# Optimization experiments

Measured on AMD Instinct MI355X. Metric: run time of the kernel, lower is better.

## Reference

```python
import jax, jax.numpy as jnp
import numpy as np

REPLACE = 4
REMAIN = 32
EPS = 1e-12


def _l2norm(x, axis):
    return x / jnp.maximum(jnp.linalg.norm(x, axis=axis, keepdims=True), EPS)


def setup_inputs() -> dict:
    key = jax.random.key(0)
    ks = jax.random.split(key, 16)
    B, d = 4096, 64
    n_users, n_entities, n_items = 100000, 200000, 50000
    K, n_cans, n_rel = 64, 64, 100
    return {
        "users": jax.random.randint(ks[0], (B,), 0, n_users),
        "items": jax.random.randint(ks[1], (B,), 0, n_items),
        "kg_neighbors": jax.random.randint(ks[2], (n_items, K), 0, n_entities),
        "all_candidates": jax.random.randint(ks[3], (n_rel, n_cans), 0, n_entities),
        "neighbor_relations": jax.random.randint(ks[4], (n_items, K), 0, n_rel),
        "user_all_embeddings": jax.random.normal(ks[5], (n_users, d), jnp.float32),
        "entity_all_embeddings": jax.random.normal(ks[6], (n_entities, d), jnp.float32),
        "item_embeddings": jax.random.normal(ks[7], (B, d), jnp.float32),
        "ui_W": jax.random.normal(ks[8], (2 * d, d), jnp.float32) / np.sqrt(2 * d),
        "ui_b": jnp.zeros((d,), jnp.float32),
        "e1_W": jax.random.normal(ks[9], (d, d), jnp.float32) / np.sqrt(d),
        "e1_b": jnp.zeros((d,), jnp.float32),
        "e2_W": jax.random.normal(ks[10], (d, d), jnp.float32) / np.sqrt(d),
        "e2_b": jnp.zeros((d,), jnp.float32),
    }


def reference(users, items, kg_neighbors, all_candidates, neighbor_relations,
              user_all_embeddings, entity_all_embeddings, item_embeddings,
              ui_W, ui_b, e1_W, e1_b, e2_W, e2_b):
    B = users.shape[0]
    d = user_all_embeddings.shape[1]
    idx_dtype = kg_neighbors.dtype

    neighbors = kg_neighbors[items]                      # [B, K]
    users_e = user_all_embeddings[users]                 # [B, d]
    ui_e = _l2norm(jnp.concatenate([users_e, item_embeddings], axis=1) @ ui_W + ui_b, 1)  # [B, d]

    # Step 1: score neighbors, pick top replace_num
    ne = _l2norm(entity_all_embeddings[neighbors] @ e1_W + e1_b, 2)   # [B, K, d]
    scores1 = jnp.einsum('bd,bkd->bk', ui_e, ne)
    logits1 = jax.nn.softmax(scores1, axis=1)
    step1_prob, step1_idx = jax.lax.top_k(logits1, REPLACE)          # [B, R]
    replaced = jnp.take_along_axis(neighbors, step1_idx, axis=1)     # [B, R]
    sel_rel = jnp.take_along_axis(neighbor_relations[items], step1_idx, axis=1)
    cf_kg1 = kg_neighbors.at[items[:, None], step1_idx].set(
        jnp.zeros((B, REPLACE), idx_dtype))
    ap1 = jnp.log(jnp.mean(step1_prob, axis=1))                      # [B]

    # Step 2: candidate pruning + sampling
    cands = all_candidates[sel_rel]                                  # [B, R, C]
    cands_e = entity_all_embeddings[cands]                           # [B, R, C, d]
    scores2 = jnp.einsum('bd,brcd->brc', users_e, cands_e)
    _, remain_idx = jax.lax.top_k(scores2, REMAIN)                   # [B, R, M]
    cands = jnp.take_along_axis(cands, remain_idx, axis=2).reshape(B * REPLACE, REMAIN)

    replaced_e = _l2norm(entity_all_embeddings[replaced] @ e1_W + e1_b, 2)
    replaced_e = replaced_e.reshape(B * REPLACE, d)
    cands_e2 = _l2norm(entity_all_embeddings[cands] @ e2_W + e2_b, 2)  # [BR, M, d]
    ui_rep = jnp.repeat(ui_e, REPLACE, axis=0)                         # [BR, d]
    s2 = jnp.einsum('nd,nmd->nm', ui_rep * replaced_e, cands_e2)       # [BR, M]
    logp2 = jax.nn.log_softmax(s2, axis=1)

    skey = jax.random.key(42)
    step2_idx = jax.random.categorical(skey, logp2, axis=1)           # [BR]
    rows = jnp.arange(B * REPLACE)
    step2_prob = jnp.exp(logp2[rows, step2_idx]).reshape(B, REPLACE)
    sel_ent = cands[rows, step2_idx].reshape(B, REPLACE)
    cf_kg2 = kg_neighbors.at[items[:, None], step1_idx].set(sel_ent.astype(idx_dtype))
    ap2 = jnp.log(jnp.mean(step1_prob, axis=1)) + jnp.log(jnp.mean(step2_prob, axis=1))
    return (cf_kg1, ap1, cf_kg2, ap2)
```

## Files before the change

kernel.cpp:

```cpp
#include <hip/hip_runtime.h>
#include <stdint.h>

#define EPS_NORM 1e-12f
#define F32_TINY 1.17549435e-38f

static __device__ __forceinline__ int rfl(int v) {
  return __builtin_amdgcn_readfirstlane(v);
}

__device__ __forceinline__ void threefry2x32(uint32_t k0, uint32_t k1,
                                             uint32_t x0, uint32_t x1,
                                             uint32_t& o0, uint32_t& o1) {
  uint32_t ks2 = k0 ^ k1 ^ 0x1BD11BDAu;
  x0 += k0; x1 += k1;
#define TF_ROT(r) { x0 += x1; x1 = (x1 << (r)) | (x1 >> (32 - (r))); x1 ^= x0; }
  TF_ROT(13) TF_ROT(15) TF_ROT(26) TF_ROT(6)
  x0 += k1; x1 += ks2 + 1u;
  TF_ROT(17) TF_ROT(29) TF_ROT(16) TF_ROT(24)
  x0 += ks2; x1 += k0 + 2u;
  TF_ROT(13) TF_ROT(15) TF_ROT(26) TF_ROT(6)
  x0 += k0; x1 += k1 + 3u;
  TF_ROT(17) TF_ROT(29) TF_ROT(16) TF_ROT(24)
  x0 += k1; x1 += ks2 + 4u;
  TF_ROT(13) TF_ROT(15) TF_ROT(26) TF_ROT(6)
  x0 += ks2; x1 += k0 + 5u;
#undef TF_ROT
  o0 = x0; o1 = x1;
}

#define PERM_IDX(p) ((((p) & 7) << 3) | ((p) >> 3))

__global__ __launch_bounds__(256) void k_phase1(
    const float* __restrict__ E, const int* __restrict__ allc,
    const float* __restrict__ W1, const float* __restrict__ b1,
    const float* __restrict__ W2, const float* __restrict__ b2,
    const float* __restrict__ U, const int* __restrict__ users,
    const float* __restrict__ Iemb, const float* __restrict__ uiW,
    const float* __restrict__ uib, const int* __restrict__ kg,
    float* __restrict__ T1, float* __restrict__ T2c,
    float* __restrict__ uiE, float* __restrict__ out0, float* __restrict__ out2,
    int* __restrict__ wkg2) {
  __shared__ float SM[8192];
  const int blk = blockIdx.x, tid = threadIdx.x;
  const int wv = tid >> 6, lane = tid & 63;
  const int NT1B = 782, NT2B = 25, NUIB = 256;
  if (blk < NT1B + NT2B) {
    const bool isT1 = blk < NT1B;
    {
      const float* W = isT1 ? W1 : W2;
      for (int idx = tid; idx < 4096; idx += 256) {
        int k = idx >> 6, c = idx & 63;
        int cg = c & 7, ci = c >> 3;
        SM[k * 64 + ((ci >> 2) * 8 + cg) * 4 + (ci & 3)] = W[idx];
      }
    }
    __syncthreads();
    const int rg = lane >> 3, cg = lane & 7;
    const int sub = lane >> 5, r = lane & 31;
    const float* bias = isT1 ? b1 : b2;
    float bv[8];
#pragma unroll
    for (int ci = 0; ci < 8; ++ci) bv[ci] = bias[ci * 8 + cg];
    float* eTw = SM + 4096 + wv * 1024;
    const float4* eT4 = reinterpret_cast<const float4*>(eTw);
    const float4* W4 = reinterpret_cast<const float4*>(SM);
#pragma unroll 1
    for (int t = 0; t < 2; ++t) {
      int batch = (isT1 ? blk : blk - NT1B) * 2 + t;
      int rbase = batch * 128 + wv * 32;
      if (isT1 && rbase >= 200000) continue;
      int srow = isT1 ? (rbase + r) : allc[rbase + r];
      const float4* Er = reinterpret_cast<const float4*>(E + (size_t)srow * 64);
      float4 a0 = Er[sub * 4 + 0], a1 = Er[sub * 4 + 1];
      float4 a2 = Er[sub * 4 + 2], a3 = Er[sub * 4 + 3];
      float4 a4 = Er[8 + sub * 4 + 0], a5 = Er[8 + sub * 4 + 1];
      float4 a6 = Er[8 + sub * 4 + 2], a7 = Er[8 + sub * 4 + 3];
      float y[4][8];
#pragma unroll
      for (int ri = 0; ri < 4; ++ri)
#pragma unroll
        for (int ci = 0; ci < 8; ++ci) y[ri][ci] = 0.f;
      {
        float ev[16] = {a0.x, a0.y, a0.z, a0.w, a1.x, a1.y, a1.z, a1.w,
                        a2.x, a2.y, a2.z, a2.w, a3.x, a3.y, a3.z, a3.w};
#pragma unroll
        for (int kk = 0; kk < 16; ++kk)
          eTw[(sub * 16 + kk) * 32 + r] = ev[kk];
#pragma unroll 8
        for (int kk = 0; kk < 32; ++kk) {
          float4 e4 = eT4[kk * 8 + rg];
          float4 wa = W4[kk * 16 + cg];
          float4 wb = W4[kk * 16 + 8 + cg];
          float ev4[4] = {e4.x, e4.y, e4.z, e4.w};
          float wv8[8] = {wa.x, wa.y, wa.z, wa.w, wb.x, wb.y, wb.z, wb.w};
#pragma unroll
          for (int ri = 0; ri < 4; ++ri)
#pragma unroll
            for (int ci = 0; ci < 8; ++ci)
              y[ri][ci] = fmaf(ev4[ri], wv8[ci], y[ri][ci]);
        }
      }
      {
        float ev[16] = {a4.x, a4.y, a4.z, a4.w, a5.x, a5.y, a5.z, a5.w,
                        a6.x, a6.y, a6.z, a6.w, a7.x, a7.y, a7.z, a7.w};
#pragma unroll
        for (int kk = 0; kk < 16; ++kk)
          eTw[(sub * 16 + kk) * 32 + r] = ev[kk];
#pragma unroll 8
        for (int kk = 0; kk < 32; ++kk) {
          float4 e4 = eT4[kk * 8 + rg];
          float4 wa = W4[(32 + kk) * 16 + cg];
          float4 wb = W4[(32 + kk) * 16 + 8 + cg];
          float ev4[4] = {e4.x, e4.y, e4.z, e4.w};
          float wv8[8] = {wa.x, wa.y, wa.z, wa.w, wb.x, wb.y, wb.z, wb.w};
#pragma unroll
          for (int ri = 0; ri < 4; ++ri)
#pragma unroll
            for (int ci = 0; ci < 8; ++ci)
              y[ri][ci] = fmaf(ev4[ri], wv8[ci], y[ri][ci]);
        }
      }
#pragma unroll
      for (int ri = 0; ri < 4; ++ri)
#pragma unroll
        for (int ci = 0; ci < 8; ++ci)
          y[ri][ci] = __fadd_rn(y[ri][ci], bv[ci]);
#pragma unroll
      for (int ri = 0; ri < 4; ++ri) {
        float A0 = __fadd_rn(__fmul_rn(y[ri][0], y[ri][0]),
                             __fmul_rn(y[ri][4], y[ri][4]));
        float A1 = __fadd_rn(__fmul_rn(y[ri][1], y[ri][1]),
                             __fmul_rn(y[ri][5], y[ri][5]));
        float A2 = __fadd_rn(__fmul_rn(y[ri][2], y[ri][2]),
                             __fmul_rn(y[ri][6], y[ri][6]));
        float A3 = __fadd_rn(__fmul_rn(y[ri][3], y[ri][3]),
                             __fmul_rn(y[ri][7], y[ri][7]));
        float B0 = __fadd_rn(A0, A2), B1 = __fadd_rn(A1, A3);
        float C = __fadd_rn(B0, B1);
        C = __fadd_rn(C, __shfl_xor(C, 4));
        C = __fadd_rn(C, __shfl_xor(C, 2));
        C = __fadd_rn(C, __shfl_xor(C, 1));
        float denom = fmaxf(sqrtf(C), EPS_NORM);
        int row = rbase + rg * 4 + ri;
        if (isT1) {
          float4* drow = reinterpret_cast<float4*>(T1 + (size_t)row * 64 + cg * 8);
          drow[0] = make_float4(y[ri][0] / denom, y[ri][1] / denom,
                                y[ri][2] / denom, y[ri][3] / denom);
          drow[1] = make_float4(y[ri][4] / denom, y[ri][5] / denom,
                                y[ri][6] / denom, y[ri][7] / denom);
        } else {
          float* drow = T2c + (size_t)row * 64;
#pragma unroll
          for (int ci = 0; ci < 8; ++ci) drow[ci * 8 + cg] = y[ri][ci] / denom;
        }
      }
    }
  } else if (blk < NT1B + NT2B + NUIB) {
    int ub = blk - (NT1B + NT2B);
    for (int i = tid; i < 8192; i += 256) SM[i] = uiW[i];
    __syncthreads();
    float bl = uib[lane];
#pragma unroll 1
    for (int t = 0; t < 4; ++t) {
      int b = ub * 16 + wv * 4 + t;
      int usr = rfl(users[b]);
      const float* ur = U + (size_t)usr * 64;
      const float* ir = Iemb + (size_t)b * 64;
      float y = 0.f;
#pragma unroll
      for (int k = 0; k < 64; ++k) y = fmaf(ur[k], SM[k * 64 + lane], y);
#pragma unroll
      for (int k = 0; k < 64; ++k) y = fmaf(ir[k], SM[(64 + k) * 64 + lane], y);
      y += bl;
      float ss = y * y;
#pragma unroll
      for (int off = 32; off; off >>= 1) ss += __shfl_xor(ss, off);
      float yn = y / fmaxf(sqrtf(ss), EPS_NORM);
      uiE[(size_t)b * 64 + lane] = yn;
    }
  } else {
    const int4* kg4 = reinterpret_cast<const int4*>(kg);
    float4* o4 = reinterpret_cast<float4*>(out0);
    float4* o24 = reinterpret_cast<float4*>(out2);
    int4* wz = reinterpret_cast<int4*>(wkg2);
    int4 z; z.x = 0; z.y = 0; z.z = 0; z.w = 0;
    for (int i = (blk - 1063) * 256 + tid; i < 800000; i += 200 * 256) {
      int4 v = kg4[i];
      float4 f = make_float4((float)v.x, (float)v.y, (float)v.z, (float)v.w);
      o4[i] = f;
      o24[i] = f;
      wz[i] = z;
    }
  }
}

__global__ __launch_bounds__(256) void k_step4(
    const int* __restrict__ items, const int* __restrict__ users,
    const int* __restrict__ kg, const int* __restrict__ nrel,
    const int* __restrict__ allc, const float* __restrict__ E,
    const float* __restrict__ T1, const float* __restrict__ T2c,
    const float* __restrict__ uiE, const float* __restrict__ U,
    float* __restrict__ out0, float* __restrict__ ap1_out,
    int* __restrict__ s1i_g, float* __restrict__ lmp1,
    float* __restrict__ p2, int* __restrict__ wkg2) {
  __shared__ int s1_idx_sh[4][4], s1_rel_sh[4][4], s1_ent_sh[4][4];
  __shared__ int kept_sh[4][32];
  const int tid = threadIdx.x, wv = tid >> 6, lane = tid & 63;
  const int blk = blockIdx.x;
  {
    const int b = blk * 4 + wv;
    const int item = rfl(items[b]);
    int nb = kg[(size_t)item * 64 + lane];
    const float4* R = reinterpret_cast<const float4*>(T1 + (size_t)nb * 64);
    float yn[64];
#pragma unroll
    for (int p4 = 0; p4 < 16; ++p4) {
      float4 v = R[p4];
      yn[PERM_IDX(4 * p4 + 0)] = v.x;
      yn[PERM_IDX(4 * p4 + 1)] = v.y;
      yn[PERM_IDX(4 * p4 + 2)] = v.z;
      yn[PERM_IDX(4 * p4 + 3)] = v.w;
    }
    const float4* Ur = reinterpret_cast<const float4*>(uiE + (size_t)b * 64);
    float D[32];
#pragma unroll
    for (int i4 = 0; i4 < 8; ++i4) {
      float4 ua = Ur[i4], ub = Ur[i4 + 8];
      float uav[4] = {ua.x, ua.y, ua.z, ua.w};
      float ubv[4] = {ub.x, ub.y, ub.z, ub.w};
#pragma unroll
      for (int t = 0; t < 4; ++t) {
        int i = i4 * 4 + t;
        D[i] = __fadd_rn(__fmul_rn(yn[i], uav[t]), __fmul_rn(yn[i + 32], ubv[t]));
      }
    }
#pragma unroll
    for (int i = 0; i < 16; ++i) D[i] = __fadd_rn(D[i], D[i + 16]);
#pragma unroll
    for (int i = 0; i < 8; ++i)  D[i] = __fadd_rn(D[i], D[i + 8]);
#pragma unroll
    for (int i = 0; i < 4; ++i)  D[i] = __fadd_rn(D[i], D[i + 4]);
#pragma unroll
    for (int i = 0; i < 2; ++i)  D[i] = __fadd_rn(D[i], D[i + 2]);
    float s = __fadd_rn(D[0], D[1]);
    float m = s;
#pragma unroll
    for (int off = 32; off; off >>= 1) m = fmaxf(m, __shfl_xor(m, off));
    float ex = expf(s - m);
    float sum = ex;
#pragma unroll
    for (int off = 32; off; off >>= 1) sum += __shfl_xor(sum, off);
    float p = ex / sum;
    int rank = 0;
    for (int k2 = 0; k2 < 64; ++k2) {
      float pv = __shfl(p, k2);
      rank += (pv > p || (pv == p && k2 < lane)) ? 1 : 0;
    }
    float acc = 0.f;
#pragma unroll
    for (int rr = 0; rr < 4; ++rr) {
      unsigned long long msk = __ballot(rank == rr);
      int src = __ffsll(msk) - 1;
      acc += __shfl(p, src);
    }
    float lm = logf(acc * 0.25f);
    if (lane == 0) { ap1_out[b] = lm; lmp1[b] = lm; }
    if (rank < 4) {
      s1_idx_sh[wv][rank] = lane;
      s1_ent_sh[wv][rank] = nb;
      s1_rel_sh[wv][rank] = nrel[(size_t)item * 64 + lane];
      s1i_g[b * 4 + rank] = lane;
      out0[(size_t)item * 64 + lane] = 0.0f;
    }
  }
  __syncthreads();
#pragma unroll 1
  for (int slot = 0; slot < 4; ++slot) {
    const int b = blk * 4 + slot;
    const int item = rfl(items[b]);
    const int n = b * 4 + wv;
    const int rel = rfl(s1_rel_sh[slot][wv]);
    const int repl = rfl(s1_ent_sh[slot][wv]);
    const int colsel = rfl(s1_idx_sh[slot][wv]);
    {
      int usr = rfl(users[b]);
      int ent = allc[rel * 64 + lane];
      const float* ur = U + (size_t)usr * 64;
      const float4* e4 = reinterpret_cast<const float4*>(E + (size_t)ent * 64);
      float s = 0.f;
#pragma unroll
      for (int j4 = 0; j4 < 16; ++j4) {
        float4 t = e4[j4];
        s = fmaf(ur[4 * j4 + 0], t.x, s);
        s = fmaf(ur[4 * j4 + 1], t.y, s);
        s = fmaf(ur[4 * j4 + 2], t.z, s);
        s = fmaf(ur[4 * j4 + 3], t.w, s);
      }
      int rank = 0;
      for (int k2 = 0; k2 < 64; ++k2) {
        float sv = __shfl(s, k2);
        rank += (sv > s || (sv == s && k2 < lane)) ? 1 : 0;
      }
      if (rank < 32) kept_sh[wv][rank] = (lane << 18) | ent;
    }
    {
      int m = lane & 31;
      int pk = kept_sh[wv][m];
      int c = pk >> 18;
      int ent = pk & 0x3FFFF;
      float q = uiE[(size_t)b * 64 + PERM_IDX(lane)] *
                T1[(size_t)repl * 64 + lane];
      const float4* c4 = reinterpret_cast<const float4*>(
          T2c + ((size_t)rel * 64 + c) * 64);
      float s = 0.f;
#pragma unroll
      for (int j4 = 0; j4 < 16; ++j4) {
        float4 t = c4[j4];
        s = fmaf(__shfl(q, PERM_IDX(4 * j4 + 0)), t.x, s);
        s = fmaf(__shfl(q, PERM_IDX(4 * j4 + 1)), t.y, s);
        s = fmaf(__shfl(q, PERM_IDX(4 * j4 + 2)), t.z, s);
        s = fmaf(__shfl(q, PERM_IDX(4 * j4 + 3)), t.w, s);
      }
      float mx = s;
#pragma unroll
      for (int off = 1; off < 32; off <<= 1) mx = fmaxf(mx, __shfl_xor(mx, off));
      float shv = s - mx;
      float se = expf(shv);
      float sum = se;
#pragma unroll
      for (int off = 1; off < 32; off <<= 1) sum += __shfl_xor(sum, off);
      float logp = shv - logf(sum);
      uint32_t h0, h1;
      threefry2x32(0u, 42u, 0u, (uint32_t)(n * 32 + m), h0, h1);
      uint32_t bits = h0 ^ h1;
      float u0 = __uint_as_float((bits >> 9) | 0x3F800000u) - 1.0f;
      float uu = fmaxf(u0, F32_TINY);
      float g = -logf(-logf(uu));
      float z = g + logp;
      float bz = z; int bm = m;
#pragma unroll
      for (int off = 1; off < 32; off <<= 1) {
        float oz = __shfl_xor(bz, off);
        int om = __shfl_xor(bm, off);
        if (oz > bz || (oz == bz && om < bm)) { bz = oz; bm = om; }
      }
      if (lane == bm) {
        p2[n] = expf(logp);
        atomicMax(&wkg2[(size_t)item * 64 + colsel], ((b + 1) << 18) | ent);
      }
    }
  }
}

__global__ __launch_bounds__(256) void k_fin2(
    const int* __restrict__ items, const int* __restrict__ s1_idx,
    const int* __restrict__ wkg2, const float* __restrict__ p2,
    const float* __restrict__ lmp1,
    float* __restrict__ out2, float* __restrict__ out3, int N, int B) {
  int i = blockIdx.x * 256 + threadIdx.x;
  if (i < N) {
    int b = i >> 2;
    int item = items[b];
    int col = s1_idx[i];
    int v = wkg2[(size_t)item * 64 + col];
    out2[(size_t)item * 64 + col] = (float)(v & 0x3FFFF);
  }
  if (i < B) {
    float a = ((p2[i * 4] + p2[i * 4 + 1]) + p2[i * 4 + 2]) + p2[i * 4 + 3];
    out3[i] = lmp1[i] + logf(a * 0.25f);
  }
}

__global__ __launch_bounds__(256) void k_init(const int* __restrict__ kg,
                                              float* __restrict__ out0,
                                              int* __restrict__ wkg2, int n) {
  int i = blockIdx.x * 256 + threadIdx.x;
  if (i < n) { int v = kg[i]; out0[i] = (float)v; wkg2[i] = v; }
}

__device__ __forceinline__ void transform_row(const float4* __restrict__ Er,
                                              const float* __restrict__ W,
                                              const float* __restrict__ bias,
                                              float (&yn)[64]) {
  float y[64];
#pragma unroll
  for (int j = 0; j < 64; ++j) y[j] = 0.f;
  float4 c0 = Er[0], c1 = Er[1], c2 = Er[2], c3 = Er[3];
#pragma unroll 1
  for (int cc = 0; cc < 4; ++cc) {
    float4 n0, n1, n2, n3;
    if (cc < 3) { n0 = Er[cc * 4 + 4]; n1 = Er[cc * 4 + 5];
                  n2 = Er[cc * 4 + 6]; n3 = Er[cc * 4 + 7]; }
    float ev[16] = {c0.x, c0.y, c0.z, c0.w, c1.x, c1.y, c1.z, c1.w,
                    c2.x, c2.y, c2.z, c2.w, c3.x, c3.y, c3.z, c3.w};
#pragma unroll
    for (int k2i = 0; k2i < 16; ++k2i) {
      const float4* Wr = reinterpret_cast<const float4*>(
          W + ((size_t)(cc * 16 + k2i)) * 64);
      float ek = ev[k2i];
#pragma unroll
      for (int j4 = 0; j4 < 16; ++j4) {
        float4 w = Wr[j4];
        y[j4 * 4 + 0] = fmaf(ek, w.x, y[j4 * 4 + 0]);
        y[j4 * 4 + 1] = fmaf(ek, w.y, y[j4 * 4 + 1]);
        y[j4 * 4 + 2] = fmaf(ek, w.z, y[j4 * 4 + 2]);
        y[j4 * 4 + 3] = fmaf(ek, w.w, y[j4 * 4 + 3]);
      }
    }
    c0 = n0; c1 = n1; c2 = n2; c3 = n3;
  }
  const float4* B4 = reinterpret_cast<const float4*>(bias);
#pragma unroll
  for (int j4 = 0; j4 < 16; ++j4) {
    float4 bb = B4[j4];
    float bv[4] = {bb.x, bb.y, bb.z, bb.w};
#pragma unroll
    for (int t = 0; t < 4; ++t) y[j4 * 4 + t] = __fadd_rn(y[j4 * 4 + t], bv[t]);
  }
  float S1[32];
#pragma unroll
  for (int i = 0; i < 32; ++i)
    S1[i] = __fadd_rn(__fmul_rn(y[i], y[i]), __fmul_rn(y[i + 32], y[i + 32]));
#pragma unroll
  for (int i = 0; i < 16; ++i) S1[i] = __fadd_rn(S1[i], S1[i + 16]);
#pragma unroll
  for (int i = 0; i < 8; ++i)  S1[i] = __fadd_rn(S1[i], S1[i + 8]);
#pragma unroll
  for (int i = 0; i < 4; ++i)  S1[i] = __fadd_rn(S1[i], S1[i + 4]);
#pragma unroll
  for (int i = 0; i < 2; ++i)  S1[i] = __fadd_rn(S1[i], S1[i + 2]);
  float ss = __fadd_rn(S1[0], S1[1]);
  float denom = fmaxf(sqrtf(ss), EPS_NORM);
#pragma unroll
  for (int j = 0; j < 64; ++j) yn[j] = y[j] / denom;
}

__global__ __launch_bounds__(256) void k_transform64(
    const float* __restrict__ src, const int* __restrict__ gidx,
    const float* __restrict__ W, const float* __restrict__ bias,
    float* __restrict__ out, int nrows) {
  __shared__ float Wl[4096];
  for (int i = threadIdx.x; i < 4096; i += 256) Wl[i] = W[i];
  __syncthreads();
  int wid = threadIdx.x >> 6, lane = threadIdx.x & 63;
  int row = rfl(blockIdx.x * 4 + wid);
  if (row >= nrows) return;
  int srow = rfl(gidx ? gidx[row] : row);
  const float* er = src + (size_t)srow * 64;
  float y = 0.f;
#pragma unroll
  for (int k = 0; k < 64; ++k) y = fmaf(er[k], Wl[k * 64 + lane], y);
  y += bias[lane];
  float ss = y * y;
#pragma unroll
  for (int off = 32; off; off >>= 1) ss += __shfl_xor(ss, off);
  float yn = y / fmaxf(sqrtf(ss), EPS_NORM);
  out[(size_t)row * 64 + lane] = yn;
}

__global__ __launch_bounds__(256) void k_ui(
    const float* __restrict__ U, const int* __restrict__ users,
    const float* __restrict__ Iemb, const float* __restrict__ W,
    const float* __restrict__ bias, float* __restrict__ out, int B) {
  __shared__ float Wl[8192];
  for (int i = threadIdx.x; i < 8192; i += 256) Wl[i] = W[i];
  __syncthreads();
  int wid = threadIdx.x >> 6, lane = threadIdx.x & 63;
  int b = rfl(blockIdx.x * 4 + wid);
  if (b >= B) return;
  int usr = rfl(users[b]);
  const float* ur = U + (size_t)usr * 64;
  const float* ir = Iemb + (size_t)b * 64;
  float y = 0.f;
#pragma unroll
  for (int k = 0; k < 64; ++k) y = fmaf(ur[k], Wl[k * 64 + lane], y);
#pragma unroll
  for (int k = 0; k < 64; ++k) y = fmaf(ir[k], Wl[(64 + k) * 64 + lane], y);
  y += bias[lane];
  float ss = y * y;
#pragma unroll
  for (int off = 32; off; off >>= 1) ss += __shfl_xor(ss, off);
  float yn = y / fmaxf(sqrtf(ss), EPS_NORM);
  out[(size_t)b * 64 + lane] = yn;
}

__device__ __forceinline__ void score1_tail(
    float s, int lane, int b, int item, int nb,
    const int* __restrict__ nrel,
    float* __restrict__ out0, float* __restrict__ ap1_out,
    int* __restrict__ s1_idx, int* __restrict__ s1_rel, int* __restrict__ s1_ent,
    float* __restrict__ lmp1, int* __restrict__ wkg2) {
  float m = s;
#pragma unroll
  for (int off = 32; off; off >>= 1) m = fmaxf(m, __shfl_xor(m, off));
  float ex = expf(s - m);
  float sum = ex;
#pragma unroll
  for (int off = 32; off; off >>= 1) sum += __shfl_xor(sum, off);
  float p = ex / sum;
  int rank = 0;
  for (int k2 = 0; k2 < 64; ++k2) {
    float pv = __shfl(p, k2);
    rank += (pv > p || (pv == p && k2 < lane)) ? 1 : 0;
  }
  float acc = 0.f;
#pragma unroll
  for (int rr = 0; rr < 4; ++rr) {
    unsigned long long msk = __ballot(rank == rr);
    int src = __ffsll(msk) - 1;
    acc += __shfl(p, src);
  }
  float lm = logf(acc * 0.25f);
  if (lane == 0) { ap1_out[b] = lm; lmp1[b] = lm; }
  if (rank < 4) {
    s1_idx[b * 4 + rank] = lane;
    s1_ent[b * 4 + rank] = nb;
    s1_rel[b * 4 + rank] = nrel[(size_t)item * 64 + lane];
    out0[(size_t)item * 64 + lane] = 0.0f;
    wkg2[(size_t)item * 64 + lane] = 0;
  }
}

__global__ __launch_bounds__(256) void k_score1(
    const int* __restrict__ items, const int* __restrict__ kg,
    const int* __restrict__ nrel, const float* __restrict__ E,
    const float* __restrict__ W1, const float* __restrict__ b1,
    const float* __restrict__ uiE,
    float* __restrict__ out0, float* __restrict__ ap1_out,
    int* __restrict__ s1_idx, int* __restrict__ s1_rel, int* __restrict__ s1_ent,
    float* __restrict__ lmp1, int* __restrict__ wkg2) {
  int tid = threadIdx.x, wv = tid >> 6, lane = tid & 63;
  int b = rfl(blockIdx.x * 4 + wv);
  int item = rfl(items[b]);
  int nb = kg[(size_t)item * 64 + lane];
  const float4* Er = reinterpret_cast<const float4*>(E + (size_t)nb * 64);
  float yn[64];
  transform_row(Er, W1, b1, yn);
  const float4* Ur = reinterpret_cast<const float4*>(uiE + (size_t)b * 64);
  float D[32];
#pragma unroll
  for (int i4 = 0; i4 < 8; ++i4) {
    float4 ua = Ur[i4], ub = Ur[i4 + 8];
    float uav[4] = {ua.x, ua.y, ua.z, ua.w};
    float ubv[4] = {ub.x, ub.y, ub.z, ub.w};
#pragma unroll
    for (int t = 0; t < 4; ++t) {
      int i = i4 * 4 + t;
      D[i] = __fadd_rn(__fmul_rn(yn[i], uav[t]), __fmul_rn(yn[i + 32], ubv[t]));
    }
  }
#pragma unroll
  for (int i = 0; i < 16; ++i) D[i] = __fadd_rn(D[i], D[i + 16]);
#pragma unroll
  for (int i = 0; i < 8; ++i)  D[i] = __fadd_rn(D[i], D[i + 8]);
#pragma unroll
  for (int i = 0; i < 4; ++i)  D[i] = __fadd_rn(D[i], D[i + 4]);
#pragma unroll
  for (int i = 0; i < 2; ++i)  D[i] = __fadd_rn(D[i], D[i + 2]);
  float s = __fadd_rn(D[0], D[1]);
  score1_tail(s, lane, b, item, nb, nrel, out0, ap1_out, s1_idx, s1_rel, s1_ent,
              lmp1, wkg2);
}

__global__ __launch_bounds__(256) void k_score2(
    const int* __restrict__ users, const int* __restrict__ s1_rel,
    const float* __restrict__ U, const float* __restrict__ E,
    const int* __restrict__ allc, int* __restrict__ kept, int N) {
  int wid = threadIdx.x >> 6, lane = threadIdx.x & 63;
  int n = rfl(blockIdx.x * 4 + wid);
  if (n >= N) return;
  int b = n >> 2;
  int rel = rfl(s1_rel[n]);
  int usr = rfl(users[b]);
  int ent = allc[rel * 64 + lane];
  const float* ur = U + (size_t)usr * 64;
  const float4* e4 = reinterpret_cast<const float4*>(E + (size_t)ent * 64);
  float s = 0.f;
#pragma unroll
  for (int j4 = 0; j4 < 16; ++j4) {
    float4 t = e4[j4];
    s = fmaf(ur[4 * j4 + 0], t.x, s);
    s = fmaf(ur[4 * j4 + 1], t.y, s);
    s = fmaf(ur[4 * j4 + 2], t.z, s);
    s = fmaf(ur[4 * j4 + 3], t.w, s);
  }
  int rank = 0;
  for (int k2 = 0; k2 < 64; ++k2) {
    float sv = __shfl(s, k2);
    rank += (sv > s || (sv == s && k2 < lane)) ? 1 : 0;
  }
  if (rank < 32) kept[n * 32 + rank] = (lane << 18) | ent;
}

template <bool PERMQ>
__device__ __forceinline__ void sample_body(
    float q, int n, int b, int lane,
    const int* __restrict__ items, const int* __restrict__ s1_idx,
    int rel, const float* __restrict__ T2c, const int* __restrict__ kept,
    float* __restrict__ p2, int* __restrict__ wkg2) {
  int m = lane & 31;
  int pk = kept[n * 32 + m];
  int c = pk >> 18;
  int ent = pk & 0x3FFFF;
  const float4* c4 = reinterpret_cast<const float4*>(T2c + ((size_t)rel * 64 + c) * 64);
  float s = 0.f;
#pragma unroll
  for (int j4 = 0; j4 < 16; ++j4) {
    float4 t = c4[j4];
    s = fmaf(__shfl(q, PERMQ ? PERM_IDX(4 * j4 + 0) : (4 * j4 + 0)), t.x, s);
    s = fmaf(__shfl(q, PERMQ ? PERM_IDX(4 * j4 + 1) : (4 * j4 + 1)), t.y, s);
    s = fmaf(__shfl(q, PERMQ ? PERM_IDX(4 * j4 + 2) : (4 * j4 + 2)), t.z, s);
    s = fmaf(__shfl(q, PERMQ ? PERM_IDX(4 * j4 + 3) : (4 * j4 + 3)), t.w, s);
  }
  float mx = s;
#pragma unroll
  for (int off = 1; off < 32; off <<= 1) mx = fmaxf(mx, __shfl_xor(mx, off));
  float shv = s - mx;
  float se = expf(shv);
  float sum = se;
#pragma unroll
  for (int off = 1; off < 32; off <<= 1) sum += __shfl_xor(sum, off);
  float logp = shv - logf(sum);
  uint32_t h0, h1;
  threefry2x32(0u, 42u, 0u, (uint32_t)(n * 32 + m), h0, h1);
  uint32_t bits = h0 ^ h1;
  float u0 = __uint_as_float((bits >> 9) | 0x3F800000u) - 1.0f;
  float uu = fmaxf(u0, F32_TINY);
  float g = -logf(-logf(uu));
  float z = g + logp;
  float bz = z; int bm = m;
#pragma unroll
  for (int off = 1; off < 32; off <<= 1) {
    float oz = __shfl_xor(bz, off);
    int om = __shfl_xor(bm, off);
    if (oz > bz || (oz == bz && om < bm)) { bz = oz; bm = om; }
  }
  if (lane == bm) {
    p2[n] = expf(logp);
    int col = s1_idx[n];
    int item = items[b];
    atomicMax(&wkg2[(size_t)item * 64 + col], ((b + 1) << 18) | ent);
  }
}

__global__ __launch_bounds__(256) void k_sample(
    const int* __restrict__ items,
    const int* __restrict__ s1_idx, const int* __restrict__ s1_rel,
    const int* __restrict__ s1_ent,
    const float* __restrict__ E, const float* __restrict__ W1,
    const float* __restrict__ b1, const float* __restrict__ T2c,
    const float* __restrict__ uiE, const int* __restrict__ kept,
    float* __restrict__ p2, int* __restrict__ wkg2, int N) {
  __shared__ float Wl[4096];
  int tid = threadIdx.x;
  for (int i = tid; i < 4096; i += 256) Wl[i] = W1[i];
  __syncthreads();
  int wid = tid >> 6, lane = tid & 63;
  int n = rfl(blockIdx.x * 4 + wid);
  if (n >= N) return;
  int b = n >> 2;
  int rel = rfl(s1_rel[n]);
  int repl = rfl(s1_ent[n]);
  const float* er = E + (size_t)repl * 64;
  float y = 0.f;
#pragma unroll
  for (int k2 = 0; k2 < 64; ++k2) y = fmaf(er[k2], Wl[k2 * 64 + lane], y);
  y += b1[lane];
  float ss = y * y;
#pragma unroll
  for (int off = 32; off; off >>= 1) ss += __shfl_xor(ss, off);
  float yn = y / fmaxf(sqrtf(ss), EPS_NORM);
  float q = uiE[(size_t)b * 64 + lane] * yn;
  sample_body<false>(q, n, b, lane, items, s1_idx, rel, T2c, kept, p2, wkg2);
}

__global__ __launch_bounds__(256) void k_fin(const int* __restrict__ wkg2,
                                             const float* __restrict__ p2,
                                             const float* __restrict__ lmp1,
                                             float* __restrict__ out2,
                                             float* __restrict__ out3,
                                             int n, int B) {
  int i = blockIdx.x * 256 + threadIdx.x;
  if (i < n) out2[i] = (float)(wkg2[i] & 0x3FFFF);
  if (i < B) {
    float a = ((p2[i * 4] + p2[i * 4 + 1]) + p2[i * 4 + 2]) + p2[i * 4 + 3];
    out3[i] = lmp1[i] + logf(a * 0.25f);
  }
}

extern "C" void kernel_launch(void* const* d_in, const int* in_sizes, int n_in,
                              void* d_out, int out_size, void* d_ws, size_t ws_size,
                              hipStream_t stream) {
  const int*   users = (const int*)d_in[0];
  const int*   items = (const int*)d_in[1];
  const int*   kg    = (const int*)d_in[2];
  const int*   allc  = (const int*)d_in[3];
  const int*   nrel  = (const int*)d_in[4];
  const float* U     = (const float*)d_in[5];
  const float* E     = (const float*)d_in[6];
  const float* Iemb  = (const float*)d_in[7];
  const float* uiW   = (const float*)d_in[8];
  const float* uib   = (const float*)d_in[9];
  const float* e1W   = (const float*)d_in[10];
  const float* e1b   = (const float*)d_in[11];
  const float* e2W   = (const float*)d_in[12];
  const float* e2b   = (const float*)d_in[13];

  const int B = 4096, NCELL = 3200000, NCAND = 6400, NR4 = 16384, NENT = 200000;

  float* out0    = (float*)d_out;
  float* out_ap1 = out0 + NCELL;
  float* out2    = out_ap1 + B;
  float* out_ap2 = out2 + NCELL;

  float* T2c  = (float*)d_ws;
  float* uiE  = T2c + 409600;
  int*   wkg2 = (int*)(uiE + 262144);
  int*   s1i  = wkg2 + NCELL;
  int*   s1r  = s1i + NR4;
  int*   s1e  = s1r + NR4;
  int*   kept = s1e + NR4;
  float* p2   = (float*)(kept + 524288);
  float* lmp1 = p2 + NR4;
  float* T1   = lmp1 + B;
  const size_t WS_NEED = ((size_t)(T1 + (size_t)NENT * 64) - (size_t)d_ws);
  const bool pathA = ws_size >= WS_NEED;

  if (pathA) {
    k_phase1<<<1263, 256, 0, stream>>>(E, allc, e1W, e1b, e2W, e2b, U, users,
                                       Iemb, uiW, uib, kg, T1, T2c, uiE,
                                       out0, out2, wkg2);
    k_step4<<<B / 4, 256, 0, stream>>>(items, users, kg, nrel, allc, E, T1, T2c,
                                       uiE, U, out0, out_ap1, s1i, lmp1, p2, wkg2);
    k_fin2<<<(NR4 + 255) / 256, 256, 0, stream>>>(items, s1i, wkg2, p2, lmp1,
                                                  out2, out_ap2, NR4, B);
  } else {
    k_init<<<(NCELL + 255) / 256, 256, 0, stream>>>(kg, out0, wkg2, NCELL);
    k_ui<<<(B + 3) / 4, 256, 0, stream>>>(U, users, Iemb, uiW, uib, uiE, B);
    k_transform64<<<(NCAND + 3) / 4, 256, 0, stream>>>(E, allc, e2W, e2b, T2c, NCAND);
    k_score1<<<B / 4, 256, 0, stream>>>(items, kg, nrel, E, e1W, e1b, uiE,
                                        out0, out_ap1, s1i, s1r, s1e, lmp1, wkg2);
    k_score2<<<(NR4 + 3) / 4, 256, 0, stream>>>(users, s1r, U, E, allc, kept, NR4);
    k_sample<<<(NR4 + 3) / 4, 256, 0, stream>>>(items, s1i, s1r, s1e, E, e1W, e1b,
                                                T2c, uiE, kept, p2, wkg2, NR4);
    k_fin<<<(NCELL + 255) / 256, 256, 0, stream>>>(wkg2, p2, lmp1, out2, out_ap2,
                                                   NCELL, B);
  }
}
```

Measured before the change: 131.9 us.

## Bucket step-2 work by relation and stage candidate embeddings in LDS

Splits the fused step kernel into a step-1 scoring kernel plus a counting sort of the (batch, replace) rows by selected relation: a count, a single-thread scan and a scatter. A new per-relation kernel then loads that relation's 64 candidate raw embeddings and transformed embeddings into swizzled LDS once and reuses them for every row with that relation. This replaces the repeated global gathers per row. It costs three extra kernel launches, atomics, and load imbalance across the 1600 blocks, since the number of rows per relation varies.

After: 188.7 us. 1.43x slower.

```diff
diff --git a/kernel.cpp b/kernel.cpp
--- a/kernel.cpp
+++ b/kernel.cpp
@@ -39,7 +39,7 @@
     const float* __restrict__ uib, const int* __restrict__ kg,
     float* __restrict__ T1, float* __restrict__ T2c,
     float* __restrict__ uiE, float* __restrict__ out0, float* __restrict__ out2,
-    int* __restrict__ wkg2) {
+    int* __restrict__ wkg2, int* __restrict__ cnt, int* __restrict__ cursor) {
   __shared__ float SM[8192];
   const int blk = blockIdx.x, tid = threadIdx.x;
   const int wv = tid >> 6, lane = tid & 63;
@@ -179,6 +179,7 @@
       uiE[(size_t)b * 64 + lane] = yn;
     }
   } else {
+    if (blk == 1063 && tid < 128) { cnt[tid] = 0; cursor[tid] = 0; }
     const int4* kg4 = reinterpret_cast<const int4*>(kg);
     float4* o4 = reinterpret_cast<float4*>(out0);
     float4* o24 = reinterpret_cast<float4*>(out2);
@@ -194,103 +195,152 @@
   }
 }
 
-__global__ __launch_bounds__(256) void k_step4(
+__global__ __launch_bounds__(256) void k_stepA(
+    const int* __restrict__ items, const int* __restrict__ kg,
+    const int* __restrict__ nrel, const float* __restrict__ T1,
+    const float* __restrict__ uiE,
+    float* __restrict__ out0, float* __restrict__ ap1_out,
+    int* __restrict__ s1i_g, int* __restrict__ s1r_g, int* __restrict__ s1e_g,
+    float* __restrict__ lmp1, int* __restrict__ cnt) {
+  const int tid = threadIdx.x, wv = tid >> 6, lane = tid & 63;
+  const int b = blockIdx.x * 4 + wv;
+  const int item = rfl(items[b]);
+  int nb = kg[(size_t)item * 64 + lane];
+  const float4* R = reinterpret_cast<const float4*>(T1 + (size_t)nb * 64);
+  float yn[64];
+#pragma unroll
+  for (int p4 = 0; p4 < 16; ++p4) {
+    float4 v = R[p4];
+    yn[PERM_IDX(4 * p4 + 0)] = v.x;
+    yn[PERM_IDX(4 * p4 + 1)] = v.y;
+    yn[PERM_IDX(4 * p4 + 2)] = v.z;
+    yn[PERM_IDX(4 * p4 + 3)] = v.w;
+  }
+  const float4* Ur = reinterpret_cast<const float4*>(uiE + (size_t)b * 64);
+  float D[32];
+#pragma unroll
+  for (int i4 = 0; i4 < 8; ++i4) {
+    float4 ua = Ur[i4], ub = Ur[i4 + 8];
+    float uav[4] = {ua.x, ua.y, ua.z, ua.w};
+    float ubv[4] = {ub.x, ub.y, ub.z, ub.w};
+#pragma unroll
+    for (int t = 0; t < 4; ++t) {
+      int i = i4 * 4 + t;
+      D[i] = __fadd_rn(__fmul_rn(yn[i], uav[t]), __fmul_rn(yn[i + 32], ubv[t]));
+    }
+  }
+#pragma unroll
+  for (int i = 0; i < 16; ++i) D[i] = __fadd_rn(D[i], D[i + 16]);
+#pragma unroll
+  for (int i = 0; i < 8; ++i)  D[i] = __fadd_rn(D[i], D[i + 8]);
+#pragma unroll
+  for (int i = 0; i < 4; ++i)  D[i] = __fadd_rn(D[i], D[i + 4]);
+#pragma unroll
+  for (int i = 0; i < 2; ++i)  D[i] = __fadd_rn(D[i], D[i + 2]);
+  float s = __fadd_rn(D[0], D[1]);
+  float m = s;
+#pragma unroll
+  for (int off = 32; off; off >>= 1) m = fmaxf(m, __shfl_xor(m, off));
+  float ex = expf(s - m);
+  float sum = ex;
+#pragma unroll
+  for (int off = 32; off; off >>= 1) sum += __shfl_xor(sum, off);
+  float p = ex / sum;
+  int rank = 0;
+  for (int k2 = 0; k2 < 64; ++k2) {
+    float pv = __shfl(p, k2);
+    rank += (pv > p || (pv == p && k2 < lane)) ? 1 : 0;
+  }
+  float acc = 0.f;
+#pragma unroll
+  for (int rr = 0; rr < 4; ++rr) {
+    unsigned long long msk = __ballot(rank == rr);
+    int src = __ffsll(msk) - 1;
+    acc += __shfl(p, src);
+  }
+  float lm = logf(acc * 0.25f);
+  if (lane == 0) { ap1_out[b] = lm; lmp1[b] = lm; }
+  if (rank < 4) {
+    int relv = nrel[(size_t)item * 64 + lane];
+    s1i_g[b * 4 + rank] = lane;
+    s1e_g[b * 4 + rank] = nb;
+    s1r_g[b * 4 + rank] = relv;
+    out0[(size_t)item * 64 + lane] = 0.0f;
+    atomicAdd(&cnt[relv], 1);
+  }
+}
+
+__global__ void k_scan(const int* __restrict__ cnt, int* __restrict__ offs) {
+  if (threadIdx.x == 0) {
+    int a = 0;
+    for (int i = 0; i < 100; ++i) { offs[i] = a; a += cnt[i]; }
+    offs[100] = a;
+  }
+}
+
+__global__ __launch_bounds__(256) void k_scatter(
+    const int* __restrict__ s1r_g, const int* __restrict__ offs,
+    int* __restrict__ cursor, int* __restrict__ order, int N) {
+  int n = blockIdx.x * 256 + threadIdx.x;
+  if (n < N) {
+    int rel = s1r_g[n];
+    int pos = atomicAdd(&cursor[rel], 1);
+    order[offs[rel] + pos] = n;
+  }
+}
+
+__global__ __launch_bounds__(256) void k_bc(
     const int* __restrict__ items, const int* __restrict__ users,
-    const int* __restrict__ kg, const int* __restrict__ nrel,
     const int* __restrict__ allc, const float* __restrict__ E,
     const float* __restrict__ T1, const float* __restrict__ T2c,
     const float* __restrict__ uiE, const float* __restrict__ U,
-    float* __restrict__ out0, float* __restrict__ ap1_out,
-    int* __restrict__ s1i_g, float* __restrict__ lmp1,
+    const int* __restrict__ s1i_g, const int* __restrict__ s1e_g,
+    const int* __restrict__ order, const int* __restrict__ offs,
     float* __restrict__ p2, int* __restrict__ wkg2) {
-  __shared__ int s1_idx_sh[4][4], s1_rel_sh[4][4], s1_ent_sh[4][4];
+  __shared__ float ELDS[4096];
+  __shared__ float TLDS[4096];
+  __shared__ int ENT[64];
   __shared__ int kept_sh[4][32];
+  const int rel = blockIdx.x >> 4, seg = blockIdx.x & 15;
   const int tid = threadIdx.x, wv = tid >> 6, lane = tid & 63;
-  const int blk = blockIdx.x;
+  const int beg = offs[rel];
+  const int cntr = offs[rel + 1] - beg;
+  if (seg * 4 >= cntr) return;
   {
-    const int b = blk * 4 + wv;
+    int c = tid >> 2, q = tid & 3;
+    int ent = allc[rel * 64 + c];
+    if (q == 0) ENT[c] = ent;
+    const float4* src = reinterpret_cast<const float4*>(E + (size_t)ent * 64);
+    const float4* srcT = reinterpret_cast<const float4*>(
+        T2c + ((size_t)rel * 64 + c) * 64);
+    float4* eld = reinterpret_cast<float4*>(ELDS);
+    float4* tld = reinterpret_cast<float4*>(TLDS);
+#pragma unroll
+    for (int t = 0; t < 4; ++t) {
+      int p4 = q * 4 + t;
+      eld[c * 16 + (p4 ^ (c & 15))] = src[p4];
+      tld[c * 16 + (p4 ^ (c & 15))] = srcT[p4];
+    }
+  }
+  __syncthreads();
+  const float4* eld = reinterpret_cast<const float4*>(ELDS);
+  const float4* tld = reinterpret_cast<const float4*>(TLDS);
+#pragma unroll 1
+  for (int i = seg * 4 + wv; i < cntr; i += 64) {
+    const int n = order[beg + i];
+    const int b = n >> 2;
     const int item = rfl(items[b]);
-    int nb = kg[(size_t)item * 64 + lane];
-    const float4* R = reinterpret_cast<const float4*>(T1 + (size_t)nb * 64);
-    float yn[64];
-#pragma unroll
-    for (int p4 = 0; p4 < 16; ++p4) {
-      float4 v = R[p4];
-      yn[PERM_IDX(4 * p4 + 0)] = v.x;
-      yn[PERM_IDX(4 * p4 + 1)] = v.y;
-      yn[PERM_IDX(4 * p4 + 2)] = v.z;
-      yn[PERM_IDX(4 * p4 + 3)] = v.w;
-    }
-    const float4* Ur = reinterpret_cast<const float4*>(uiE + (size_t)b * 64);
-    float D[32];
-#pragma unroll
-    for (int i4 = 0; i4 < 8; ++i4) {
-      float4 ua = Ur[i4], ub = Ur[i4 + 8];
-      float uav[4] = {ua.x, ua.y, ua.z, ua.w};
-      float ubv[4] = {ub.x, ub.y, ub.z, ub.w};
-#pragma unroll
-      for (int t = 0; t < 4; ++t) {
-        int i = i4 * 4 + t;
-        D[i] = __fadd_rn(__fmul_rn(yn[i], uav[t]), __fmul_rn(yn[i + 32], ubv[t]));
-      }
-    }
-#pragma unroll
-    for (int i = 0; i < 16; ++i) D[i] = __fadd_rn(D[i], D[i + 16]);
-#pragma unroll
-    for (int i = 0; i < 8; ++i)  D[i] = __fadd_rn(D[i], D[i + 8]);
-#pragma unroll
-    for (int i = 0; i < 4; ++i)  D[i] = __fadd_rn(D[i], D[i + 4]);
-#pragma unroll
-    for (int i = 0; i < 2; ++i)  D[i] = __fadd_rn(D[i], D[i + 2]);
-    float s = __fadd_rn(D[0], D[1]);
-    float m = s;
-#pragma unroll
-    for (int off = 32; off; off >>= 1) m = fmaxf(m, __shfl_xor(m, off));
-    float ex = expf(s - m);
-    float sum = ex;
-#pragma unroll
-    for (int off = 32; off; off >>= 1) sum += __shfl_xor(sum, off);
-    float p = ex / sum;
-    int rank = 0;
-    for (int k2 = 0; k2 < 64; ++k2) {
-      float pv = __shfl(p, k2);
-      rank += (pv > p || (pv == p && k2 < lane)) ? 1 : 0;
-    }
-    float acc = 0.f;
-#pragma unroll
-    for (int rr = 0; rr < 4; ++rr) {
-      unsigned long long msk = __ballot(rank == rr);
-      int src = __ffsll(msk) - 1;
-      acc += __shfl(p, src);
-    }
-    float lm = logf(acc * 0.25f);
-    if (lane == 0) { ap1_out[b] = lm; lmp1[b] = lm; }
-    if (rank < 4) {
-      s1_idx_sh[wv][rank] = lane;
-      s1_ent_sh[wv][rank] = nb;
-      s1_rel_sh[wv][rank] = nrel[(size_t)item * 64 + lane];
-      s1i_g[b * 4 + rank] = lane;
-      out0[(size_t)item * 64 + lane] = 0.0f;
-    }
-  }
-  __syncthreads();
-#pragma unroll 1
-  for (int slot = 0; slot < 4; ++slot) {
-    const int b = blk * 4 + slot;
-    const int item = rfl(items[b]);
-    const int n = b * 4 + wv;
-    const int rel = rfl(s1_rel_sh[slot][wv]);
-    const int repl = rfl(s1_ent_sh[slot][wv]);
-    const int colsel = rfl(s1_idx_sh[slot][wv]);
+    const int repl = rfl(s1e_g[n]);
+    const int colsel = rfl(s1i_g[n]);
+    int kept_pk;
     {
       int usr = rfl(users[b]);
-      int ent = allc[rel * 64 + lane];
+      int ent = ENT[lane];
       const float* ur = U + (size_t)usr * 64;
-      const float4* e4 = reinterpret_cast<const float4*>(E + (size_t)ent * 64);
       float s = 0.f;
 #pragma unroll
       for (int j4 = 0; j4 < 16; ++j4) {
-        float4 t = e4[j4];
+        float4 t = eld[lane * 16 + (j4 ^ (lane & 15))];
         s = fmaf(ur[4 * j4 + 0], t.x, s);
         s = fmaf(ur[4 * j4 + 1], t.y, s);
         s = fmaf(ur[4 * j4 + 2], t.z, s);
@@ -302,20 +352,19 @@
         rank += (sv > s || (sv == s && k2 < lane)) ? 1 : 0;
       }
       if (rank < 32) kept_sh[wv][rank] = (lane << 18) | ent;
+      kept_pk = kept_sh[wv][lane & 31];
     }
     {
       int m = lane & 31;
-      int pk = kept_sh[wv][m];
+      int pk = kept_pk;
       int c = pk >> 18;
       int ent = pk & 0x3FFFF;
       float q = uiE[(size_t)b * 64 + PERM_IDX(lane)] *
                 T1[(size_t)repl * 64 + lane];
-      const float4* c4 = reinterpret_cast<const float4*>(
-          T2c + ((size_t)rel * 64 + c) * 64);
       float s = 0.f;
 #pragma unroll
       for (int j4 = 0; j4 < 16; ++j4) {
-        float4 t = c4[j4];
+        float4 t = tld[c * 16 + (j4 ^ (c & 15))];
         s = fmaf(__shfl(q, PERM_IDX(4 * j4 + 0)), t.x, s);
         s = fmaf(__shfl(q, PERM_IDX(4 * j4 + 1)), t.y, s);
         s = fmaf(__shfl(q, PERM_IDX(4 * j4 + 2)), t.z, s);
@@ -722,16 +771,24 @@
   int*   kept = s1e + NR4;
   float* p2   = (float*)(kept + 524288);
   float* lmp1 = p2 + NR4;
-  float* T1   = lmp1 + B;
+  int*   cnt    = (int*)(lmp1 + B);
+  int*   offs   = cnt + 128;
+  int*   cursor = offs + 128;
+  float* T1   = (float*)(cursor + 128);
+  int*   order = kept;
   const size_t WS_NEED = ((size_t)(T1 + (size_t)NENT * 64) - (size_t)d_ws);
   const bool pathA = ws_size >= WS_NEED;
 
   if (pathA) {
     k_phase1<<<1263, 256, 0, stream>>>(E, allc, e1W, e1b, e2W, e2b, U, users,
                                        Iemb, uiW, uib, kg, T1, T2c, uiE,
-                                       out0, out2, wkg2);
-    k_step4<<<B / 4, 256, 0, stream>>>(items, users, kg, nrel, allc, E, T1, T2c,
-                                       uiE, U, out0, out_ap1, s1i, lmp1, p2, wkg2);
+                                       out0, out2, wkg2, cnt, cursor);
+    k_stepA<<<B / 4, 256, 0, stream>>>(items, kg, nrel, T1, uiE,
+                                       out0, out_ap1, s1i, s1r, s1e, lmp1, cnt);
+    k_scan<<<1, 64, 0, stream>>>(cnt, offs);
+    k_scatter<<<(NR4 + 255) / 256, 256, 0, stream>>>(s1r, offs, cursor, order, NR4);
+    k_bc<<<100 * 16, 256, 0, stream>>>(items, users, allc, E, T1, T2c, uiE, U,
+                                       s1i, s1e, order, offs, p2, wkg2);
     k_fin2<<<(NR4 + 255) / 256, 256, 0, stream>>>(items, s1i, wkg2, p2, lmp1,
                                                   out2, out_ap2, NR4, B);
   } else {
```
